# Optimization experiments

Measured on AMD Instinct MI355X. Metric: run time of the kernel, lower is better.

Reference implementation:

```python
import jax, jax.numpy as jnp
import numpy as np

B, T, E, H, V = 64, 256, 300, 512, 50000
G = 3 * H  # gates: r, z, n (PyTorch order)


def setup_inputs() -> dict:
    key = jax.random.key(0)
    ks = jax.random.split(key, 14)
    k = 1.0 / np.sqrt(H)
    u = lambda kk, sh: jax.random.uniform(kk, sh, jnp.float32, -k, k)
    x = jax.random.randint(ks[0], (B, T), 0, V)
    emb = jax.random.normal(ks[1], (V, E), jnp.float32) * 0.1
    emb = emb.at[0].set(0.0)  # padding_idx=0
    return {
        "x": x,
        "emb": emb,
        # layer 0: input E, both directions stacked on axis 0
        "w_ih0": u(ks[2], (2, G, E)),
        "w_hh0": u(ks[3], (2, G, H)),
        "b_ih0": u(ks[4], (2, G)),
        "b_hh0": u(ks[5], (2, G)),
        # layer 1: input 2H
        "w_ih1": u(ks[6], (2, G, 2 * H)),
        "w_hh1": u(ks[7], (2, G, 2 * H if False else H)) if False else u(ks[7], (2, G, H)),
        "b_ih1": u(ks[8], (2, G)),
        "b_hh1": u(ks[9], (2, G)),
        # classifier
        "w1": u(ks[10], (128, 2 * H)),
        "b1": u(ks[11], (128,)),
        "w2": u(ks[12], (2, 128)),
        "b2": u(ks[13], (2,)),
    }


def _gru_dir(x, w_ih, w_hh, b_ih, b_hh, reverse):
    # x: [B, T, in]; precompute input projections for all timesteps
    xp = jnp.einsum('bti,gi->btg', x, w_ih) + b_ih  # [B, T, 3H]

    def step(h, xp_t):
        gh = h @ w_hh.T + b_hh  # [B, 3H]
        r = jax.nn.sigmoid(xp_t[:, :H] + gh[:, :H])
        z = jax.nn.sigmoid(xp_t[:, H:2 * H] + gh[:, H:2 * H])
        n = jnp.tanh(xp_t[:, 2 * H:] + r * gh[:, 2 * H:])
        h = (1.0 - z) * n + z * h
        return h, h

    h0 = jnp.zeros((x.shape[0], H), x.dtype)
    _, ys = jax.lax.scan(step, h0, jnp.swapaxes(xp, 0, 1), reverse=reverse)
    return jnp.swapaxes(ys, 0, 1)  # [B, T, H], aligned to input positions


def _bigru_layer(x, w_ih, w_hh, b_ih, b_hh):
    f = _gru_dir(x, w_ih[0], w_hh[0], b_ih[0], b_hh[0], False)
    b = _gru_dir(x, w_ih[1], w_hh[1], b_ih[1], b_hh[1], True)
    return jnp.concatenate([f, b], axis=-1)  # [B, T, 2H]


def reference(x, emb, w_ih0, w_hh0, b_ih0, b_hh0, w_ih1, w_hh1, b_ih1, b_hh1, w1, b1, w2, b2):
    e = emb[x]  # [B, T, E]
    h = _bigru_layer(e, w_ih0, w_hh0, b_ih0, b_hh0)
    h = _bigru_layer(h, w_ih1, w_hh1, b_ih1, b_hh1)  # dropout=eval mode (identity)
    pooled = jnp.max(h, axis=1)  # [B, 2H]
    hid = jax.nn.relu(pooled @ w1.T + b1)
    return hid @ w2.T + b2  # [B, 2]
```

## Files before the change

kernel.cpp:

```cpp
#include <hip/hip_runtime.h>

#define BB 64
#define TLEN 256
#define HH 512
#define GG 1536
#define EPAD 320
#define NN 3072
#define MM 16384

typedef __attribute__((ext_vector_type(8))) __fp16 half8;
typedef __attribute__((ext_vector_type(4))) __fp16 half4;
typedef __attribute__((ext_vector_type(4))) float floatx4;

typedef union { unsigned long long u[2]; half8 v; } hpack;
typedef union { half4 h4; unsigned long long u; } hpack4;

__global__ __launch_bounds__(256) void g2_embed(const int* __restrict__ x,
                                                const float* __restrict__ emb,
                                                __fp16* __restrict__ e) {
  int idx = blockIdx.x * 256 + threadIdx.x;
  int row = idx / 80;
  int c = idx - row * 80;
  int t = row >> 6, b = row & 63;
  half4 v = {0, 0, 0, 0};
  if (c < 75) {
    int xi = x[b * TLEN + t];
    float4 f = *(const float4*)&emb[(long)xi * 300 + c * 4];
    v[0] = (__fp16)f.x; v[1] = (__fp16)f.y; v[2] = (__fp16)f.z; v[3] = (__fp16)f.w;
  }
  *(half4*)&e[row * EPAD + c * 4] = v;
}

__global__ __launch_bounds__(256) void g2_padw(const float* __restrict__ w,
                                               __fp16* __restrict__ wp) {
  int idx = blockIdx.x * 256 + threadIdx.x;
  int row = idx / 80;
  int c = idx - row * 80;
  half4 v = {0, 0, 0, 0};
  if (c < 75) {
    float4 f = *(const float4*)&w[(long)row * 300 + c * 4];
    v[0] = (__fp16)f.x; v[1] = (__fp16)f.y; v[2] = (__fp16)f.z; v[3] = (__fp16)f.w;
  }
  *(half4*)&wp[row * EPAD + c * 4] = v;
}

__global__ __launch_bounds__(256) void g2_cvt(const float* __restrict__ src,
                                              __fp16* __restrict__ dst) {
  long idx = (long)blockIdx.x * 256 + threadIdx.x;
  float4 a = *(const float4*)&src[idx * 8];
  float4 b = *(const float4*)&src[idx * 8 + 4];
  half8 o;
  o[0] = (__fp16)a.x; o[1] = (__fp16)a.y; o[2] = (__fp16)a.z; o[3] = (__fp16)a.w;
  o[4] = (__fp16)b.x; o[5] = (__fp16)b.y; o[6] = (__fp16)b.z; o[7] = (__fp16)b.w;
  *(half8*)&dst[idx * 8] = o;
}

__global__ __launch_bounds__(256) void g2_gemm(const __fp16* __restrict__ A,
                                               const __fp16* __restrict__ W,
                                               const float* __restrict__ bias,
                                               __fp16* __restrict__ C,
                                               int M, int N, int Kp) {
  __shared__ __fp16 As[128][72];
  __shared__ __fp16 Ws[128][72];
  const int nTiles = N >> 7;
  const int m0 = (blockIdx.x / nTiles) << 7;
  const int n0 = (blockIdx.x % nTiles) << 7;
  const int tid = threadIdx.x;
  const int lane = tid & 63, wv = tid >> 6;
  const int wm = (wv >> 1) << 6, wn = (wv & 1) << 6;
  const int nsub = lane & 15, quad = lane >> 4;

  floatx4 acc[4][4];
#pragma unroll
  for (int i = 0; i < 4; i++)
#pragma unroll
    for (int j = 0; j < 4; j++) acc[i][j] = (floatx4){0.f, 0.f, 0.f, 0.f};

  const int lr = tid >> 3;
  const int lc = (tid & 7) << 3;
  for (int ko = 0; ko < Kp; ko += 64) {
#pragma unroll
    for (int p = 0; p < 4; p++) {
      int r = lr + p * 32;
      *(half8*)&As[r][lc] = *(const half8*)&A[(long)(m0 + r) * Kp + ko + lc];
      *(half8*)&Ws[r][lc] = *(const half8*)&W[(long)(n0 + r) * Kp + ko + lc];
    }
    __syncthreads();
#pragma unroll
    for (int kk = 0; kk < 64; kk += 32) {
      half8 af[4], bf[4];
      const int kr = kk + (quad << 3);
#pragma unroll
      for (int i = 0; i < 4; i++) af[i] = *(const half8*)&As[wm + i * 16 + nsub][kr];
#pragma unroll
      for (int j = 0; j < 4; j++) bf[j] = *(const half8*)&Ws[wn + j * 16 + nsub][kr];
#pragma unroll
      for (int i = 0; i < 4; i++)
#pragma unroll
        for (int j = 0; j < 4; j++)
          acc[i][j] = __builtin_amdgcn_mfma_f32_16x16x32_f16(af[i], bf[j], acc[i][j], 0, 0, 0);
    }
    __syncthreads();
  }
#pragma unroll
  for (int j = 0; j < 4; j++) {
    int col = n0 + wn + j * 16 + nsub;
    float bv = bias[col];
#pragma unroll
    for (int i = 0; i < 4; i++) {
      int rb = m0 + wm + i * 16 + (quad << 2);
#pragma unroll
      for (int ii = 0; ii < 4; ii++)
        C[(long)(rb + ii) * N + col] = (__fp16)(acc[i][j][ii] + bv);
    }
  }
}

__global__ __launch_bounds__(256, 1) void g2_rnn(const float* __restrict__ whh,
                                                 const float* __restrict__ bhh,
                                                 const __fp16* __restrict__ xp,
                                                 __fp16* __restrict__ hout,
                                                 __fp16* __restrict__ hx) {
  __shared__ __fp16 Wl[96][520];
  __shared__ __fp16 hst[4][16][20];
  const unsigned long long SENT = 0xFFFFFFFFFFFFFFFFULL;
  const int bid = blockIdx.x;
  const int gi = bid & 3;
  const int uo = bid >> 2;
  const int d = gi >> 1, g = gi & 1;
  const int tid = threadIdx.x;
  const int lane = tid & 63, wv = tid >> 6;
  const int U0 = uo << 5;
  const int mb = wv & 1, ut = wv >> 1;
  const int nsub = lane & 15, quad = lane >> 4;
  const int bq = (g << 5) + (mb << 4);
  const int ul = (ut << 4) + nsub;

  const float* wd = whh + (long)d * (GG * HH);
  for (int idx = tid; idx < 96 * 64; idx += 256) {
    int r = idx >> 6;
    int c = (idx & 63) << 3;
    int gate = r >> 5, u2 = r & 31;
    const float* src = &wd[(long)(gate * HH + U0 + u2) * HH + c];
    float4 a = *(const float4*)&src[0];
    float4 b = *(const float4*)&src[4];
    half8 o;
    o[0] = (__fp16)a.x; o[1] = (__fp16)a.y; o[2] = (__fp16)a.z; o[3] = (__fp16)a.w;
    o[4] = (__fp16)b.x; o[5] = (__fp16)b.y; o[6] = (__fp16)b.z; o[7] = (__fp16)b.w;
    *(half8*)&Wl[r][c] = o;
  }
  __syncthreads();

  half8 wr_[16], wz_[16], wn_[16];
#pragma unroll
  for (int kk = 0; kk < 16; kk++) {
    const int kcol = (kk << 5) + (quad << 3);
    wr_[kk] = *(const half8*)&Wl[ul][kcol];
    wz_[kk] = *(const half8*)&Wl[32 + ul][kcol];
    wn_[kk] = *(const half8*)&Wl[64 + ul][kcol];
  }

  const float bhr = bhh[d * GG + U0 + ul];
  const float bhz = bhh[d * GG + HH + U0 + ul];
  const float bhn = bhh[d * GG + 2 * HH + U0 + ul];

  const int cidx = ((quad >> 1) << 6) + (nsub << 2) + ((quad & 1) << 1);
  const int pr = lane & 15, pc4 = (lane >> 4) << 2;
  const int pidx = (uo << 7) + (ut << 6) + (pr << 2) + (pc4 >> 2);

  float hprev[4] = {0.f, 0.f, 0.f, 0.f};

  for (int s = 0; s < TLEN; s++) {
    const int tt = d ? (TLEN - 1 - s) : s;
    float xr[4], xz[4], xn[4];
    {
      const __fp16* xb0 = xp + (long)(tt * BB) * NN + d * GG + U0 + ul;
#pragma unroll
      for (int i = 0; i < 4; i++) {
        const __fp16* xb = xb0 + (long)(bq + (quad << 2) + i) * NN;
        xr[i] = (float)xb[0];
        xz[i] = (float)xb[HH];
        xn[i] = (float)xb[2 * HH];
      }
    }
    floatx4 ar = {0.f, 0.f, 0.f, 0.f}, az = ar, an = ar;
    if (s > 0) {
      const int pt = d ? (tt + 1) : (tt - 1);
      const unsigned long long* hx8 =
          (const unsigned long long*)(hx + ((((long)pt * 2 + d) * 2 + g) * 2 + mb) * 8192);
      hpack u[16];
      unsigned inv = 0xFFFFFFFFu;
      do {
#pragma unroll
        for (int kk = 0; kk < 16; kk++) {
          if (inv & (1u << (2 * kk)))
            u[kk].u[0] = __hip_atomic_load(&hx8[kk * 128 + cidx], __ATOMIC_RELAXED, __HIP_MEMORY_SCOPE_AGENT);
          if (inv & (1u << (2 * kk + 1)))
            u[kk].u[1] = __hip_atomic_load(&hx8[kk * 128 + cidx + 1], __ATOMIC_RELAXED, __HIP_MEMORY_SCOPE_AGENT);
        }
        unsigned ninv = 0;
#pragma unroll
        for (int kk = 0; kk < 16; kk++) {
          ninv |= (u[kk].u[0] == SENT) ? (1u << (2 * kk)) : 0u;
          ninv |= (u[kk].u[1] == SENT) ? (1u << (2 * kk + 1)) : 0u;
        }
        inv = ninv;
      } while (__any(inv != 0));
#pragma unroll
      for (int kk = 0; kk < 16; kk++) {
        ar = __builtin_amdgcn_mfma_f32_16x16x32_f16(u[kk].v, wr_[kk], ar, 0, 0, 0);
        az = __builtin_amdgcn_mfma_f32_16x16x32_f16(u[kk].v, wz_[kk], az, 0, 0, 0);
        an = __builtin_amdgcn_mfma_f32_16x16x32_f16(u[kk].v, wn_[kk], an, 0, 0, 0);
      }
    }
#pragma unroll
    for (int i = 0; i < 4; i++) {
      float grv = ar[i] + xr[i] + bhr;
      float gzv = az[i] + xz[i] + bhz;
      float gnv = an[i] + bhn;
      float rg = 1.f / (1.f + __expf(-grv));
      float zg = 1.f / (1.f + __expf(-gzv));
      float ex = __expf(2.f * (xn[i] + rg * gnv));
      float ng = 1.f - 2.f / (ex + 1.f);
      float hv = (1.f - zg) * ng + zg * hprev[i];
      hprev[i] = hv;
      hst[wv][(quad << 2) + i][nsub] = (__fp16)hv;
    }
    asm volatile("" ::: "memory");
    {
      hpack4 pk;
      pk.h4 = *(const half4*)&hst[wv][pr][pc4];
      unsigned long long* hxw =
          (unsigned long long*)(hx + ((((long)tt * 2 + d) * 2 + g) * 2 + mb) * 8192);
      __hip_atomic_store(&hxw[pidx], pk.u, __ATOMIC_RELAXED, __HIP_MEMORY_SCOPE_AGENT);
      *(half4*)&hout[(long)(tt * BB + (g << 5) + (mb << 4) + pr) * 1024 +
                     d * HH + U0 + (ut << 4) + pc4] = pk.h4;
    }
  }
}

__global__ __launch_bounds__(256) void g2_pool(const __fp16* __restrict__ h1,
                                               float* __restrict__ pooled) {
  int b = blockIdx.x;
  int j0 = threadIdx.x * 4;
  float m[4] = {-3e38f, -3e38f, -3e38f, -3e38f};
  const __fp16* p = h1 + b * 1024 + j0;
  for (int t = 0; t < TLEN; t++) {
    half4 v = *(const half4*)(p + (long)t * BB * 1024);
#pragma unroll
    for (int q = 0; q < 4; q++) m[q] = fmaxf(m[q], (float)v[q]);
  }
  float* o = pooled + b * 1024 + j0;
#pragma unroll
  for (int q = 0; q < 4; q++) o[q] = m[q];
}

__global__ __launch_bounds__(128) void g2_head(const float* __restrict__ pooled,
                                               const float* __restrict__ w1,
                                               const float* __restrict__ b1,
                                               const float* __restrict__ w2,
                                               const float* __restrict__ b2,
                                               float* __restrict__ out) {
  __shared__ float pl[1024];
  __shared__ float hid[128];
  int b = blockIdx.x, j = threadIdx.x;
  for (int k = j; k < 1024; k += 128) pl[k] = pooled[b * 1024 + k];
  __syncthreads();
  float acc = b1[j];
  const float* wr = w1 + (long)j * 1024;
  for (int k = 0; k < 1024; k += 4) {
    float4 w = *(const float4*)&wr[k];
    acc += pl[k] * w.x + pl[k + 1] * w.y + pl[k + 2] * w.z + pl[k + 3] * w.w;
  }
  hid[j] = fmaxf(acc, 0.f);
  __syncthreads();
  if (j < 2) {
    float a = b2[j];
    for (int k = 0; k < 128; k++) a += hid[k] * w2[j * 128 + k];
    out[b * 2 + j] = a;
  }
}

extern "C" void kernel_launch(void* const* d_in, const int* in_sizes, int n_in,
                              void* d_out, int out_size, void* d_ws, size_t ws_size,
                              hipStream_t stream) {
  (void)in_sizes; (void)n_in; (void)out_size; (void)ws_size;
  const int* x = (const int*)d_in[0];
  const float* emb = (const float*)d_in[1];
  const float* w_ih0 = (const float*)d_in[2];
  const float* w_hh0 = (const float*)d_in[3];
  const float* b_ih0 = (const float*)d_in[4];
  const float* b_hh0 = (const float*)d_in[5];
  const float* w_ih1 = (const float*)d_in[6];
  const float* w_hh1 = (const float*)d_in[7];
  const float* b_ih1 = (const float*)d_in[8];
  const float* b_hh1 = (const float*)d_in[9];
  const float* w1 = (const float*)d_in[10];
  const float* b1 = (const float*)d_in[11];
  const float* w2 = (const float*)d_in[12];
  const float* b2 = (const float*)d_in[13];

  char* ws = (char*)d_ws;
  __fp16* xp = (__fp16*)(ws + 0);
  __fp16* h0 = (__fp16*)(ws + 100663296);
  __fp16* h1 = (__fp16*)(ws + 134217728);
  __fp16* e_pad = (__fp16*)(ws + 167772160);
  __fp16* w0p = (__fp16*)(ws + 178257920);
  __fp16* w1c = (__fp16*)(ws + 180224000);
  float* pooled = (float*)(ws + 186515456);

  (void)hipMemsetAsync(h1, 0xFF, 33554432, stream);
  g2_embed<<<5120, 256, 0, stream>>>(x, emb, e_pad);
  g2_padw<<<960, 256, 0, stream>>>(w_ih0, w0p);
  g2_cvt<<<1536, 256, 0, stream>>>(w_ih1, w1c);
  g2_gemm<<<3072, 256, 0, stream>>>(e_pad, w0p, b_ih0, xp, MM, NN, EPAD);
  g2_rnn<<<64, 256, 0, stream>>>(w_hh0, b_hh0, xp, h0, h1);
  g2_gemm<<<3072, 256, 0, stream>>>(h0, w1c, b_ih1, xp, MM, NN, 1024);
  (void)hipMemsetAsync(h0, 0xFF, 33554432, stream);
  g2_rnn<<<64, 256, 0, stream>>>(w_hh1, b_hh1, xp, h1, h0);
  g2_pool<<<64, 256, 0, stream>>>(h1, pooled);
  g2_head<<<64, 128, 0, stream>>>(pooled, w1, b1, w2, b2, (float*)d_out);
}
```

Measured before the change: 2.175 ms.

## Prefetch next hidden state early, split MFMA accumulators, merge prep kernels

The recurrent kernel now issues the loads of the next step's hidden-state slice right after publishing its own output. The sentinel check then runs only on the already-loaded values, and it re-polls only when some of them are still unwritten. The MFMA chain is split into two independent accumulators per gate to shorten the dependent latency chain. The three preprocessing kernels are also fused into one launch to save launch overhead. The risk is that the early loads often still see the sentinel and need extra polling rounds, and the extra accumulators raise register pressure.

```diff
diff --git a/kernel.cpp b/kernel.cpp
--- a/kernel.cpp
+++ b/kernel.cpp
@@ -15,44 +15,45 @@
 typedef union { unsigned long long u[2]; half8 v; } hpack;
 typedef union { half4 h4; unsigned long long u; } hpack4;
 
-__global__ __launch_bounds__(256) void g2_embed(const int* __restrict__ x,
-                                                const float* __restrict__ emb,
-                                                __fp16* __restrict__ e) {
-  int idx = blockIdx.x * 256 + threadIdx.x;
-  int row = idx / 80;
-  int c = idx - row * 80;
-  int t = row >> 6, b = row & 63;
-  half4 v = {0, 0, 0, 0};
-  if (c < 75) {
-    int xi = x[b * TLEN + t];
-    float4 f = *(const float4*)&emb[(long)xi * 300 + c * 4];
-    v[0] = (__fp16)f.x; v[1] = (__fp16)f.y; v[2] = (__fp16)f.z; v[3] = (__fp16)f.w;
-  }
-  *(half4*)&e[row * EPAD + c * 4] = v;
-}
-
-__global__ __launch_bounds__(256) void g2_padw(const float* __restrict__ w,
-                                               __fp16* __restrict__ wp) {
-  int idx = blockIdx.x * 256 + threadIdx.x;
-  int row = idx / 80;
-  int c = idx - row * 80;
-  half4 v = {0, 0, 0, 0};
-  if (c < 75) {
-    float4 f = *(const float4*)&w[(long)row * 300 + c * 4];
-    v[0] = (__fp16)f.x; v[1] = (__fp16)f.y; v[2] = (__fp16)f.z; v[3] = (__fp16)f.w;
-  }
-  *(half4*)&wp[row * EPAD + c * 4] = v;
-}
-
-__global__ __launch_bounds__(256) void g2_cvt(const float* __restrict__ src,
-                                              __fp16* __restrict__ dst) {
-  long idx = (long)blockIdx.x * 256 + threadIdx.x;
-  float4 a = *(const float4*)&src[idx * 8];
-  float4 b = *(const float4*)&src[idx * 8 + 4];
-  half8 o;
-  o[0] = (__fp16)a.x; o[1] = (__fp16)a.y; o[2] = (__fp16)a.z; o[3] = (__fp16)a.w;
-  o[4] = (__fp16)b.x; o[5] = (__fp16)b.y; o[6] = (__fp16)b.z; o[7] = (__fp16)b.w;
-  *(half8*)&dst[idx * 8] = o;
+__global__ __launch_bounds__(256) void g2_prep(const int* __restrict__ x,
+                                               const float* __restrict__ emb,
+                                               __fp16* __restrict__ e,
+                                               const float* __restrict__ w_ih0,
+                                               __fp16* __restrict__ w0p,
+                                               const float* __restrict__ w_ih1,
+                                               __fp16* __restrict__ w1c) {
+  const int blk = blockIdx.x;
+  if (blk < 960) {
+    int idx = blk * 256 + threadIdx.x;
+    int row = idx / 80;
+    int c = idx - row * 80;
+    half4 v = {0, 0, 0, 0};
+    if (c < 75) {
+      float4 f = *(const float4*)&w_ih0[(long)row * 300 + c * 4];
+      v[0] = (__fp16)f.x; v[1] = (__fp16)f.y; v[2] = (__fp16)f.z; v[3] = (__fp16)f.w;
+    }
+    *(half4*)&w0p[row * EPAD + c * 4] = v;
+  } else if (blk < 2496) {
+    long idx = (long)(blk - 960) * 256 + threadIdx.x;
+    float4 a = *(const float4*)&w_ih1[idx * 8];
+    float4 b = *(const float4*)&w_ih1[idx * 8 + 4];
+    half8 o;
+    o[0] = (__fp16)a.x; o[1] = (__fp16)a.y; o[2] = (__fp16)a.z; o[3] = (__fp16)a.w;
+    o[4] = (__fp16)b.x; o[5] = (__fp16)b.y; o[6] = (__fp16)b.z; o[7] = (__fp16)b.w;
+    *(half8*)&w1c[idx * 8] = o;
+  } else {
+    int idx = (blk - 2496) * 256 + threadIdx.x;
+    int row = idx / 80;
+    int c = idx - row * 80;
+    int t = row >> 6, b = row & 63;
+    half4 v = {0, 0, 0, 0};
+    if (c < 75) {
+      int xi = x[b * TLEN + t];
+      float4 f = *(const float4*)&emb[(long)xi * 300 + c * 4];
+      v[0] = (__fp16)f.x; v[1] = (__fp16)f.y; v[2] = (__fp16)f.z; v[3] = (__fp16)f.w;
+    }
+    *(half4*)&e[row * EPAD + c * 4] = v;
+  }
 }
 
 __global__ __launch_bounds__(256) void g2_gemm(const __fp16* __restrict__ A,
@@ -169,6 +170,7 @@
   const int pidx = (uo << 7) + (ut << 6) + (pr << 2) + (pc4 >> 2);
 
   float hprev[4] = {0.f, 0.f, 0.f, 0.f};
+  hpack u[16];
 
   for (int s = 0; s < TLEN; s++) {
     const int tt = d ? (TLEN - 1 - s) : s;
@@ -183,14 +185,18 @@
         xn[i] = (float)xb[2 * HH];
       }
     }
-    floatx4 ar = {0.f, 0.f, 0.f, 0.f}, az = ar, an = ar;
+    floatx4 ar0 = {0.f, 0.f, 0.f, 0.f}, ar1 = ar0, az0 = ar0, az1 = ar0, an0 = ar0, an1 = ar0;
     if (s > 0) {
       const int pt = d ? (tt + 1) : (tt - 1);
       const unsigned long long* hx8 =
           (const unsigned long long*)(hx + ((((long)pt * 2 + d) * 2 + g) * 2 + mb) * 8192);
-      hpack u[16];
-      unsigned inv = 0xFFFFFFFFu;
-      do {
+      unsigned inv = 0;
+#pragma unroll
+      for (int kk = 0; kk < 16; kk++) {
+        inv |= (u[kk].u[0] == SENT) ? (1u << (2 * kk)) : 0u;
+        inv |= (u[kk].u[1] == SENT) ? (1u << (2 * kk + 1)) : 0u;
+      }
+      while (__any(inv != 0)) {
 #pragma unroll
         for (int kk = 0; kk < 16; kk++) {
           if (inv & (1u << (2 * kk)))
@@ -205,19 +211,22 @@
           ninv |= (u[kk].u[1] == SENT) ? (1u << (2 * kk + 1)) : 0u;
         }
         inv = ninv;
-      } while (__any(inv != 0));
-#pragma unroll
-      for (int kk = 0; kk < 16; kk++) {
-        ar = __builtin_amdgcn_mfma_f32_16x16x32_f16(u[kk].v, wr_[kk], ar, 0, 0, 0);
-        az = __builtin_amdgcn_mfma_f32_16x16x32_f16(u[kk].v, wz_[kk], az, 0, 0, 0);
-        an = __builtin_amdgcn_mfma_f32_16x16x32_f16(u[kk].v, wn_[kk], an, 0, 0, 0);
+      }
+#pragma unroll
+      for (int kk = 0; kk < 16; kk += 2) {
+        ar0 = __builtin_amdgcn_mfma_f32_16x16x32_f16(u[kk].v, wr_[kk], ar0, 0, 0, 0);
+        az0 = __builtin_amdgcn_mfma_f32_16x16x32_f16(u[kk].v, wz_[kk], az0, 0, 0, 0);
+        an0 = __builtin_amdgcn_mfma_f32_16x16x32_f16(u[kk].v, wn_[kk], an0, 0, 0, 0);
+        ar1 = __builtin_amdgcn_mfma_f32_16x16x32_f16(u[kk + 1].v, wr_[kk + 1], ar1, 0, 0, 0);
+        az1 = __builtin_amdgcn_mfma_f32_16x16x32_f16(u[kk + 1].v, wz_[kk + 1], az1, 0, 0, 0);
+        an1 = __builtin_amdgcn_mfma_f32_16x16x32_f16(u[kk + 1].v, wn_[kk + 1], an1, 0, 0, 0);
       }
     }
 #pragma unroll
     for (int i = 0; i < 4; i++) {
-      float grv = ar[i] + xr[i] + bhr;
-      float gzv = az[i] + xz[i] + bhz;
-      float gnv = an[i] + bhn;
+      float grv = ar0[i] + ar1[i] + xr[i] + bhr;
+      float gzv = az0[i] + az1[i] + xz[i] + bhz;
+      float gnv = an0[i] + an1[i] + bhn;
       float rg = 1.f / (1.f + __expf(-grv));
       float zg = 1.f / (1.f + __expf(-gzv));
       float ex = __expf(2.f * (xn[i] + rg * gnv));
@@ -235,6 +244,15 @@
       __hip_atomic_store(&hxw[pidx], pk.u, __ATOMIC_RELAXED, __HIP_MEMORY_SCOPE_AGENT);
       *(half4*)&hout[(long)(tt * BB + (g << 5) + (mb << 4) + pr) * 1024 +
                      d * HH + U0 + (ut << 4) + pc4] = pk.h4;
+    }
+    if (s + 1 < TLEN) {
+      const unsigned long long* hx8n =
+          (const unsigned long long*)(hx + ((((long)tt * 2 + d) * 2 + g) * 2 + mb) * 8192);
+#pragma unroll
+      for (int kk = 0; kk < 16; kk++) {
+        u[kk].u[0] = __hip_atomic_load(&hx8n[kk * 128 + cidx], __ATOMIC_RELAXED, __HIP_MEMORY_SCOPE_AGENT);
+        u[kk].u[1] = __hip_atomic_load(&hx8n[kk * 128 + cidx + 1], __ATOMIC_RELAXED, __HIP_MEMORY_SCOPE_AGENT);
+      }
     }
   }
 }
@@ -310,9 +328,7 @@
   float* pooled = (float*)(ws + 186515456);
 
   (void)hipMemsetAsync(h1, 0xFF, 33554432, stream);
-  g2_embed<<<5120, 256, 0, stream>>>(x, emb, e_pad);
-  g2_padw<<<960, 256, 0, stream>>>(w_ih0, w0p);
-  g2_cvt<<<1536, 256, 0, stream>>>(w_ih1, w1c);
+  g2_prep<<<7616, 256, 0, stream>>>(x, emb, e_pad, w_ih0, w0p, w_ih1, w1c);
   g2_gemm<<<3072, 256, 0, stream>>>(e_pad, w0p, b_ih0, xp, MM, NN, EPAD);
   g2_rnn<<<64, 256, 0, stream>>>(w_hh0, b_hh0, xp, h0, h1);
   g2_gemm<<<3072, 256, 0, stream>>>(h0, w1c, b_ih1, xp, MM, NN, 1024);
```

Result: slower. 3.268 ms (+50.3%).
